# Performance work log

Hardware: AMD Instinct MI355X
Metric: run time of the kernel (lower is better)

The kernel has to match this reference:

```python
import jax, jax.numpy as jnp
import numpy as np

M_MODES = 12
N_PHOTONS = 6  # input_state = [1]*6 + [0]*6


def _glynn_signs(n):
    # All delta in {+1,-1}^n with delta_0 = +1 : 2^(n-1) sign vectors.
    k = np.arange(2 ** (n - 1))
    bits = (k[:, None] >> np.arange(n - 1)[None, :]) & 1  # [S, n-1]
    signs = np.concatenate([np.ones((k.size, 1)), 1.0 - 2.0 * bits], axis=1)
    parity = np.prod(signs, axis=1)  # [S]
    return jnp.asarray(signs, jnp.float32), jnp.asarray(parity, jnp.float32)


def _batched_permanent(Msub):
    # Glynn formula: perm(M) = 2^(1-n) * sum_delta prod(delta) * prod_j sum_i delta_i M_ij
    n = Msub.shape[-1]
    signs, parity = _glynn_signs(n)
    signs = signs.astype(Msub.dtype)
    # [..., S, n] row-sums under each sign vector
    rowsums = jnp.einsum('sn,...nj->...sj', signs, Msub)
    prods = jnp.prod(rowsums, axis=-1)  # [..., S]
    perm = jnp.einsum('s,...s->...', parity.astype(Msub.dtype), prods)
    return perm / (2.0 ** (n - 1))


def _feature_unitaries(x, A, B):
    # U(x) = A @ diag(exp(i x)) @ B  (phase-shifter layer between fixed interferometers)
    ph = jnp.exp(1j * x.astype(jnp.complex64))  # [N, m]
    return jnp.einsum('ab,nb,bc->nac', A, ph, B)  # [N, m, m]


def setup_inputs() -> dict:
    key = jax.random.key(0)
    k1, k2, k3, k4 = jax.random.split(key, 4)
    x1 = jax.random.normal(k1, (384, M_MODES), jnp.float32)
    x2 = jax.random.normal(k2, (384, M_MODES), jnp.float32)
    # Fixed Haar-random unitaries for the interferometer meshes
    rng = np.random.default_rng(0)
    A = np.linalg.qr(rng.normal(size=(M_MODES, M_MODES)) + 1j * rng.normal(size=(M_MODES, M_MODES)))[0]
    B = np.linalg.qr(rng.normal(size=(M_MODES, M_MODES)) + 1j * rng.normal(size=(M_MODES, M_MODES)))[0]
    return {
        'x1': x1, 'x2': x2,
        'A_re': jnp.asarray(A.real, jnp.float32), 'A_im': jnp.asarray(A.imag, jnp.float32),
        'B_re': jnp.asarray(B.real, jnp.float32), 'B_im': jnp.asarray(B.imag, jnp.float32),
    }


def reference(x1, x2, A_re, A_im, B_re, B_im):
    A = (A_re + 1j * A_im).astype(jnp.complex64)
    B = (B_re + 1j * B_im).astype(jnp.complex64)
    U1 = _feature_unitaries(x1, A, B)  # [N1, m, m]
    U2 = _feature_unitaries(x2, A, B)  # [N2, m, m]
    n = N_PHOTONS
    # W = U(x2)^dag U(x1); amplitude = perm(W[s_idx, s_idx]) with s_idx = first n modes
    # (input_state = [1]*n + [0]*(m-n), all factorials = 1)
    Wsub = jnp.einsum('jka,ikb->ijab', jnp.conj(U2[:, :, :n]), U1[:, :, :n])  # [N1,N2,n,n]
    amp = _batched_permanent(Wsub)  # [N1, N2] complex
    K = jnp.abs(amp) ** 2
    return K.astype(jnp.float32)
```

## Files before the change

kernel.cpp:

```cpp
#include <hip/hip_runtime.h>


typedef float v2f __attribute__((ext_vector_type(2)));

#define NS 384
#define MM 12
#define NP 6
#define TS 16
#define SV_STRIDE 148

__device__ __forceinline__ v2f cmul(v2f a, v2f b) {
    v2f r = (v2f){a.x, a.x} * b;
    return __builtin_elementwise_fma((v2f){a.y, a.y}, (v2f){-b.y, b.x}, r);
}
__device__ __forceinline__ v2f cmac(v2f acc, v2f a, v2f b) {
    acc = __builtin_elementwise_fma((v2f){a.x, a.x}, b, acc);
    return __builtin_elementwise_fma((v2f){a.y, a.y}, (v2f){-b.y, b.x}, acc);
}

__global__ void build_V_kernel(const float* __restrict__ x1,
                               const float* __restrict__ x2,
                               const float* __restrict__ Ar, const float* __restrict__ Ai,
                               const float* __restrict__ Br, const float* __restrict__ Bi,
                               float* __restrict__ V1, float* __restrict__ V2c) {
    int idx = blockIdx.x * blockDim.x + threadIdx.x;
    if (idx >= 2 * NS * MM * NP) return;
    int c = idx % NP;  int rest = idx / NP;
    int a = rest % MM; rest /= MM;
    int s = rest % NS; int half = rest / NS;
    const float* x = half ? x2 : x1;

    v2f u = {0.f, 0.f};
#pragma unroll
    for (int b = 0; b < MM; ++b) {
        float sv, cv;
        __sincosf(x[s * MM + b], &sv, &cv);
        v2f ph = {cv, sv};
        v2f Bv = {Br[b * MM + c], Bi[b * MM + c]};
        v2f t  = cmul(ph, Bv);
        v2f Av = {Ar[a * MM + b], Ai[a * MM + b]};
        u = cmac(u, Av, t);
    }
    float* V = half ? V2c : V1;
    int off = ((s * MM + a) * NP + c) * 2;
    V[off]     = u.x;
    V[off + 1] = half ? -u.y : u.y;
}

__device__ __forceinline__ v2f tree_prod(const v2f rs[NP]) {
    v2f p01 = cmul(rs[0], rs[1]);
    v2f p23 = cmul(rs[2], rs[3]);
    v2f p45 = cmul(rs[4], rs[5]);
    return cmul(cmul(p01, p23), p45);
}

__global__ __launch_bounds__(256) void perm_kernel(const float* __restrict__ V1g,
                                                   const float* __restrict__ V2g,
                                                   float* __restrict__ out) {
    __shared__ __align__(16) float sV1[TS * SV_STRIDE];
    __shared__ __align__(16) float sV2[TS * SV_STRIDE];
    const int i0 = blockIdx.y * TS;
    const int j0 = blockIdx.x * TS;
    const int tid = threadIdx.x;

    for (int idx = tid; idx < 2 * TS * 36; idx += 256) {
        int which = idx >= TS * 36;
        int rem = which ? idx - TS * 36 : idx;
        int s = rem / 36, q = rem - s * 36;
        const float* src = which ? (V2g + (j0 + s) * 144) : (V1g + (i0 + s) * 144);
        float4 v = *(const float4*)(src + q * 4);
        float* dst = (which ? sV2 : sV1) + s * SV_STRIDE + q * 4;
        *(float4*)dst = v;
    }
    __syncthreads();

    const int tx = tid & 15, ty = tid >> 4;
    const float* v1 = sV1 + ty * SV_STRIDE;
    const float* v2 = sV2 + tx * SV_STRIDE;

    v2f W[NP][NP];
#pragma unroll
    for (int a = 0; a < NP; ++a)
#pragma unroll
        for (int b = 0; b < NP; ++b) W[a][b] = (v2f){0.f, 0.f};

#pragma unroll
    for (int k = 0; k < MM; ++k) {
        const v2f* c1 = (const v2f*)(v1 + k * 12);
        const v2f* c2 = (const v2f*)(v2 + k * 12);
        v2f a1[NP], a2[NP];
#pragma unroll
        for (int b = 0; b < NP; ++b) { a1[b] = c1[b]; a2[b] = c2[b]; }
#pragma unroll
        for (int a = 0; a < NP; ++a)
#pragma unroll
            for (int b = 0; b < NP; ++b)
                W[a][b] = cmac(W[a][b], a2[a], a1[b]);
    }

    v2f base[NP];
#pragma unroll
    for (int b = 0; b < NP; ++b) {
        base[b] = W[0][b];
#pragma unroll
        for (int a = 1; a < NP; ++a) base[b] += W[a][b];
    }

    v2f rs[4][NP];
#pragma unroll
    for (int b = 0; b < NP; ++b) {
        v2f m2 = {-2.f, -2.f};
        rs[0][b] = base[b];
        rs[1][b] = __builtin_elementwise_fma(m2, W[4][b], base[b]);
        rs[2][b] = __builtin_elementwise_fma(m2, W[5][b], base[b]);
        rs[3][b] = __builtin_elementwise_fma(m2, W[5][b], rs[1][b]);
    }
    v2f acc[4];
#pragma unroll
    for (int ch = 0; ch < 4; ++ch) acc[ch] = tree_prod(rs[ch]);

    unsigned st = 0;
#pragma unroll
    for (int u = 1; u < 8; ++u) {
        const int bitpos = __builtin_ctz(u);
        const int r = bitpos + 1;
        float cf = ((st >> bitpos) & 1) ? 2.f : -2.f;
        st ^= (1u << bitpos);
        float sgn_u = (u & 1) ? -1.f : 1.f;
        v2f cfv = {cf, cf};
        v2f sgv = {sgn_u, sgn_u};
#pragma unroll
        for (int ch = 0; ch < 4; ++ch) {
#pragma unroll
            for (int b = 0; b < NP; ++b)
                rs[ch][b] = __builtin_elementwise_fma(cfv, W[r][b], rs[ch][b]);
            v2f p = tree_prod(rs[ch]);
            acc[ch] = __builtin_elementwise_fma(sgv, p, acc[ch]);
        }
    }

    v2f aa = acc[0] - acc[1] - acc[2] + acc[3];
    float K = fmaf(aa.x, aa.x, aa.y * aa.y) * (1.f / 1024.f);
    out[(i0 + ty) * NS + (j0 + tx)] = K;
}

extern "C" void kernel_launch(void* const* d_in, const int* in_sizes, int n_in,
                              void* d_out, int out_size, void* d_ws, size_t ws_size,
                              hipStream_t stream) {
    const float* x1 = (const float*)d_in[0];
    const float* x2 = (const float*)d_in[1];
    const float* Ar = (const float*)d_in[2];
    const float* Ai = (const float*)d_in[3];
    const float* Br = (const float*)d_in[4];
    const float* Bi = (const float*)d_in[5];
    float* out = (float*)d_out;

    float* V1  = (float*)d_ws;
    float* V2c = V1 + NS * MM * NP * 2;

    int total = 2 * NS * MM * NP;
    build_V_kernel<<<(total + 255) / 256, 256, 0, stream>>>(x1, x2, Ar, Ai, Br, Bi, V1, V2c);

    dim3 grid(NS / TS, NS / TS);
    perm_kernel<<<grid, 256, 0, stream>>>(V1, V2c, out);
}
```

Measured before the change: 78.49 us.

## Split each permanent across two lanes with shuffle reductions

Each output element is now computed by a pair of threads. Each lane does half of the k-reduction for the 6x6 W matrix and half of the Glynn sign-chain work (two chains instead of four). Partial results are combined with xor-shuffles. The tile becomes 8x16 outputs per block, so the grid has twice as many blocks, and launch bounds now request 4 blocks per SM. The goal is to cut per-thread register pressure and latency while raising parallelism, at the cost of extra shuffles and some duplicated base and shared-memory work.

Measured after the change: 79.10 us. No clear change (+0.8%).

```diff
diff --git a/kernel.cpp b/kernel.cpp
--- a/kernel.cpp
+++ b/kernel.cpp
@@ -6,7 +6,8 @@
 #define NS 384
 #define MM 12
 #define NP 6
-#define TS 16
+#define TSJ 16
+#define TSI 8
 #define SV_STRIDE 148
 
 __device__ __forceinline__ v2f cmul(v2f a, v2f b) {
@@ -54,18 +55,18 @@
     return cmul(cmul(p01, p23), p45);
 }
 
-__global__ __launch_bounds__(256) void perm_kernel(const float* __restrict__ V1g,
-                                                   const float* __restrict__ V2g,
-                                                   float* __restrict__ out) {
-    __shared__ __align__(16) float sV1[TS * SV_STRIDE];
-    __shared__ __align__(16) float sV2[TS * SV_STRIDE];
-    const int i0 = blockIdx.y * TS;
-    const int j0 = blockIdx.x * TS;
+__global__ __launch_bounds__(256, 4) void perm_kernel(const float* __restrict__ V1g,
+                                                      const float* __restrict__ V2g,
+                                                      float* __restrict__ out) {
+    __shared__ __align__(16) float sV1[TSI * SV_STRIDE];
+    __shared__ __align__(16) float sV2[TSJ * SV_STRIDE];
+    const int i0 = blockIdx.y * TSI;
+    const int j0 = blockIdx.x * TSJ;
     const int tid = threadIdx.x;
 
-    for (int idx = tid; idx < 2 * TS * 36; idx += 256) {
-        int which = idx >= TS * 36;
-        int rem = which ? idx - TS * 36 : idx;
+    for (int idx = tid; idx < (TSI + TSJ) * 36; idx += 256) {
+        int which = idx >= TSI * 36;
+        int rem = which ? idx - TSI * 36 : idx;
         int s = rem / 36, q = rem - s * 36;
         const float* src = which ? (V2g + (j0 + s) * 144) : (V1g + (i0 + s) * 144);
         float4 v = *(const float4*)(src + q * 4);
@@ -74,7 +75,10 @@
     }
     __syncthreads();
 
-    const int tx = tid & 15, ty = tid >> 4;
+    const int h  = tid & 1;
+    const int p  = tid >> 1;
+    const int tx = p & 15;
+    const int ty = p >> 4;
     const float* v1 = sV1 + ty * SV_STRIDE;
     const float* v2 = sV2 + tx * SV_STRIDE;
 
@@ -85,7 +89,8 @@
         for (int b = 0; b < NP; ++b) W[a][b] = (v2f){0.f, 0.f};
 
 #pragma unroll
-    for (int k = 0; k < MM; ++k) {
+    for (int kk = 0; kk < NP; ++kk) {
+        const int k = h * NP + kk;
         const v2f* c1 = (const v2f*)(v1 + k * 12);
         const v2f* c2 = (const v2f*)(v2 + k * 12);
         v2f a1[NP], a2[NP];
@@ -98,6 +103,16 @@
                 W[a][b] = cmac(W[a][b], a2[a], a1[b]);
     }
 
+#pragma unroll
+    for (int a = 0; a < NP; ++a)
+#pragma unroll
+        for (int b = 0; b < NP; ++b) {
+            v2f w = W[a][b];
+            w.x += __shfl_xor(w.x, 1);
+            w.y += __shfl_xor(w.y, 1);
+            W[a][b] = w;
+        }
+
     v2f base[NP];
 #pragma unroll
     for (int b = 0; b < NP; ++b) {
@@ -106,18 +121,18 @@
         for (int a = 1; a < NP; ++a) base[b] += W[a][b];
     }
 
-    v2f rs[4][NP];
+    const float hf = -2.f * (float)h;
+    v2f rs[2][NP];
 #pragma unroll
     for (int b = 0; b < NP; ++b) {
-        v2f m2 = {-2.f, -2.f};
-        rs[0][b] = base[b];
-        rs[1][b] = __builtin_elementwise_fma(m2, W[4][b], base[b]);
-        rs[2][b] = __builtin_elementwise_fma(m2, W[5][b], base[b]);
-        rs[3][b] = __builtin_elementwise_fma(m2, W[5][b], rs[1][b]);
+        v2f r0 = __builtin_elementwise_fma((v2f){hf, hf}, W[5][b], base[b]);
+        rs[0][b] = r0;
+        rs[1][b] = __builtin_elementwise_fma((v2f){-2.f, -2.f}, W[4][b], r0);
     }
-    v2f acc[4];
+
+    v2f acc[2];
 #pragma unroll
-    for (int ch = 0; ch < 4; ++ch) acc[ch] = tree_prod(rs[ch]);
+    for (int ch = 0; ch < 2; ++ch) acc[ch] = tree_prod(rs[ch]);
 
     unsigned st = 0;
 #pragma unroll
@@ -130,18 +145,24 @@
         v2f cfv = {cf, cf};
         v2f sgv = {sgn_u, sgn_u};
 #pragma unroll
-        for (int ch = 0; ch < 4; ++ch) {
+        for (int ch = 0; ch < 2; ++ch) {
 #pragma unroll
             for (int b = 0; b < NP; ++b)
                 rs[ch][b] = __builtin_elementwise_fma(cfv, W[r][b], rs[ch][b]);
-            v2f p = tree_prod(rs[ch]);
-            acc[ch] = __builtin_elementwise_fma(sgv, p, acc[ch]);
+            v2f pr = tree_prod(rs[ch]);
+            acc[ch] = __builtin_elementwise_fma(sgv, pr, acc[ch]);
         }
     }
 
-    v2f aa = acc[0] - acc[1] - acc[2] + acc[3];
-    float K = fmaf(aa.x, aa.x, aa.y * aa.y) * (1.f / 1024.f);
-    out[(i0 + ty) * NS + (j0 + tx)] = K;
+    float psgn = h ? -1.f : 1.f;
+    v2f at = (acc[0] - acc[1]) * (v2f){psgn, psgn};
+    at.x += __shfl_xor(at.x, 1);
+    at.y += __shfl_xor(at.y, 1);
+
+    if (h == 0) {
+        float K = fmaf(at.x, at.x, at.y * at.y) * (1.f / 1024.f);
+        out[(i0 + ty) * NS + (j0 + tx)] = K;
+    }
 }
 
 extern "C" void kernel_launch(void* const* d_in, const int* in_sizes, int n_in,
@@ -161,6 +182,6 @@
     int total = 2 * NS * MM * NP;
     build_V_kernel<<<(total + 255) / 256, 256, 0, stream>>>(x1, x2, Ar, Ai, Br, Bi, V1, V2c);
 
-    dim3 grid(NS / TS, NS / TS);
+    dim3 grid(NS / TSJ, NS / TSI);
     perm_kernel<<<grid, 256, 0, stream>>>(V1, V2c, out);
 }
```

## Fuse feature-unitary construction into permanent kernel, drop workspace pass

Applied to the files above, without the earlier changes.

Removes the separate build_V kernel and computes each block's 16+16 rows of U(x)[:, :6] directly into shared memory inside the permanent kernel. This eliminates one kernel launch and the global round trip through the workspace. In exchange, every block recomputes its unitary rows: 24x redundant sincos and complex matmul work per sample across the grid. Only 192 of 256 threads do this prologue, and each does a serial 12x12 loop.

New measurement: 78.05 us. About the same (-0.6%).

```diff
diff --git a/kernel.cpp b/kernel.cpp
--- a/kernel.cpp
+++ b/kernel.cpp
@@ -18,35 +18,6 @@
     return __builtin_elementwise_fma((v2f){a.y, a.y}, (v2f){-b.y, b.x}, acc);
 }
 
-__global__ void build_V_kernel(const float* __restrict__ x1,
-                               const float* __restrict__ x2,
-                               const float* __restrict__ Ar, const float* __restrict__ Ai,
-                               const float* __restrict__ Br, const float* __restrict__ Bi,
-                               float* __restrict__ V1, float* __restrict__ V2c) {
-    int idx = blockIdx.x * blockDim.x + threadIdx.x;
-    if (idx >= 2 * NS * MM * NP) return;
-    int c = idx % NP;  int rest = idx / NP;
-    int a = rest % MM; rest /= MM;
-    int s = rest % NS; int half = rest / NS;
-    const float* x = half ? x2 : x1;
-
-    v2f u = {0.f, 0.f};
-#pragma unroll
-    for (int b = 0; b < MM; ++b) {
-        float sv, cv;
-        __sincosf(x[s * MM + b], &sv, &cv);
-        v2f ph = {cv, sv};
-        v2f Bv = {Br[b * MM + c], Bi[b * MM + c]};
-        v2f t  = cmul(ph, Bv);
-        v2f Av = {Ar[a * MM + b], Ai[a * MM + b]};
-        u = cmac(u, Av, t);
-    }
-    float* V = half ? V2c : V1;
-    int off = ((s * MM + a) * NP + c) * 2;
-    V[off]     = u.x;
-    V[off + 1] = half ? -u.y : u.y;
-}
-
 __device__ __forceinline__ v2f tree_prod(const v2f rs[NP]) {
     v2f p01 = cmul(rs[0], rs[1]);
     v2f p23 = cmul(rs[2], rs[3]);
@@ -54,23 +25,47 @@
     return cmul(cmul(p01, p23), p45);
 }
 
-__global__ __launch_bounds__(256) void perm_kernel(const float* __restrict__ V1g,
-                                                   const float* __restrict__ V2g,
-                                                   float* __restrict__ out) {
+__global__ __launch_bounds__(256) void fused_kernel(const float* __restrict__ x1,
+                                                    const float* __restrict__ x2,
+                                                    const float* __restrict__ Ar,
+                                                    const float* __restrict__ Ai,
+                                                    const float* __restrict__ Br,
+                                                    const float* __restrict__ Bi,
+                                                    float* __restrict__ out) {
     __shared__ __align__(16) float sV1[TS * SV_STRIDE];
     __shared__ __align__(16) float sV2[TS * SV_STRIDE];
     const int i0 = blockIdx.y * TS;
     const int j0 = blockIdx.x * TS;
     const int tid = threadIdx.x;
 
-    for (int idx = tid; idx < 2 * TS * 36; idx += 256) {
-        int which = idx >= TS * 36;
-        int rem = which ? idx - TS * 36 : idx;
-        int s = rem / 36, q = rem - s * 36;
-        const float* src = which ? (V2g + (j0 + s) * 144) : (V1g + (i0 + s) * 144);
-        float4 v = *(const float4*)(src + q * 4);
-        float* dst = (which ? sV2 : sV1) + s * SV_STRIDE + q * 4;
-        *(float4*)dst = v;
+    if (tid < 2 * TS * NP) {
+        int sm = tid / NP, c = tid - sm * NP;
+        int half = sm >= TS;
+        int s = half ? (j0 + sm - TS) : (i0 + sm);
+        const float* x = half ? x2 : x1;
+
+        v2f t[MM];
+#pragma unroll
+        for (int b = 0; b < MM; ++b) {
+            float sv, cv;
+            __sincosf(x[s * MM + b], &sv, &cv);
+            v2f Bv = {Br[b * MM + c], Bi[b * MM + c]};
+            t[b] = cmul((v2f){cv, sv}, Bv);
+        }
+
+        float* dst = (half ? sV2 : sV1) + (sm & (TS - 1)) * SV_STRIDE;
+        float sgn = half ? -1.f : 1.f;
+#pragma unroll
+        for (int a = 0; a < MM; ++a) {
+            v2f u = {0.f, 0.f};
+#pragma unroll
+            for (int b = 0; b < MM; ++b) {
+                v2f Av = {Ar[a * MM + b], Ai[a * MM + b]};
+                u = cmac(u, Av, t[b]);
+            }
+            dst[(a * NP + c) * 2]     = u.x;
+            dst[(a * NP + c) * 2 + 1] = sgn * u.y;
+        }
     }
     __syncthreads();
 
@@ -154,13 +149,8 @@
     const float* Br = (const float*)d_in[4];
     const float* Bi = (const float*)d_in[5];
     float* out = (float*)d_out;
-
-    float* V1  = (float*)d_ws;
-    float* V2c = V1 + NS * MM * NP * 2;
-
-    int total = 2 * NS * MM * NP;
-    build_V_kernel<<<(total + 255) / 256, 256, 0, stream>>>(x1, x2, Ar, Ai, Br, Bi, V1, V2c);
+    (void)d_ws; (void)ws_size;
 
     dim3 grid(NS / TS, NS / TS);
-    perm_kernel<<<grid, 256, 0, stream>>>(V1, V2c, out);
+    fused_kernel<<<grid, 256, 0, stream>>>(x1, x2, Ar, Ai, Br, Bi, out);
 }
```
